# Kernel optimization log

Hardware: AMD Instinct MI355X
Metric: run time of the kernel (lower is better)

Reference implementation:

```python
import jax, jax.numpy as jnp
import numpy as np

B, L, D, H = 4, 2048, 1024, 16
DH = D // H
THETA = 100000.0


def setup_inputs() -> dict:
    key = jax.random.key(0)
    k1, k2, k3 = jax.random.split(key, 3)
    std_w = (2.0 / (D + 3 * D)) ** 0.5
    std_o = (2.0 / (D + D)) ** 0.5
    return {
        "x": jax.random.normal(k1, (B, L, D), dtype=jnp.float32),
        "W": jax.random.normal(k2, (3 * D, D), dtype=jnp.float32) * std_w,
        "Wo": jax.random.normal(k3, (D, D), dtype=jnp.float32) * std_o,
    }


def _rope(t):
    # t: [B, H, L, DH]; interleaved pair rotation as in the torch module
    pos = jnp.arange(L, dtype=jnp.float32)
    inv_freq = 1.0 / THETA ** (jnp.arange(0, DH, 2, dtype=jnp.float32) / DH)
    ang = pos[:, None] * inv_freq[None, :]            # [L, DH/2]
    cos = jnp.cos(ang)[:, :, None]                    # [L, DH/2, 1]
    sin = jnp.sin(ang)[:, :, None]
    tp = t.reshape(*t.shape[:-1], DH // 2, 2)         # pairs (x1, x2)
    x1, x2 = tp[..., 0], tp[..., 1]
    rot = jnp.stack([-x2, x1], axis=-1)               # [-x2, x1]
    out = tp * cos + rot * sin
    return out.reshape(*t.shape)


def reference(x, W, Wo):
    # fused QKV projection: weight layout is (t h d) along output dim
    qkv = jnp.einsum('bld,ed->ble', x, W)             # [B, L, 3D]
    qkv = qkv.reshape(B, L, 3, H, DH)
    qkv = jnp.transpose(qkv, (0, 3, 1, 2, 4))         # [B, H, L, 3, DH]
    Q, K, V = qkv[..., 0, :], qkv[..., 1, :], qkv[..., 2, :]
    Q, K = _rope(Q), _rope(K)
    scores = jnp.einsum('bhqd,bhkd->bhqk', Q, K) / (DH ** 0.5)
    causal = jnp.tril(jnp.ones((L, L), dtype=bool))
    scores = jnp.where(causal, scores, -jnp.inf)
    attn = jax.nn.softmax(scores, axis=-1)
    out = jnp.einsum('bhqk,bhkd->bhqd', attn, V)      # [B, H, L, DH]
    out = jnp.transpose(out, (0, 2, 1, 3)).reshape(B, L, D)
    return jnp.einsum('bld,ed->ble', out, Wo)
```

## Files before the change

### kernel.cpp

```cpp
#include <hip/hip_runtime.h>
#include <cstddef>
#include <cstdint>


typedef unsigned short u16;
typedef short bf16x8 __attribute__((ext_vector_type(8)));
typedef float f32x4 __attribute__((ext_vector_type(4)));

#define B_   4
#define L_   2048
#define H_   16
#define DH_  64
#define D_   1024
#define E3_  3072

__device__ __forceinline__ u16 f2bf(float f) {
  unsigned int u = __float_as_uint(f);
  u += 0x7fffu + ((u >> 16) & 1u);
  return (u16)(u >> 16);
}
__device__ __forceinline__ float bf2f(u16 h) {
  return __uint_as_float(((unsigned int)h) << 16);
}
__device__ __forceinline__ unsigned pk2(float a, float b) {
  return ((__float_as_uint(a) + 0x8000u) >> 16) |
         ((__float_as_uint(b) + 0x8000u) & 0xffff0000u);
}
__device__ __forceinline__ float fexp2(float x) {
#if __has_builtin(__builtin_amdgcn_exp2f)
  return __builtin_amdgcn_exp2f(x);
#else
  return exp2f(x);
#endif
}

__device__ __forceinline__ void gload_lds16(const void* g, void* l) {
  auto gp = reinterpret_cast<const uint32_t __attribute__((address_space(1)))*>(
      reinterpret_cast<uintptr_t>(g));
  auto lp = reinterpret_cast<uint32_t __attribute__((address_space(3)))*>(
      reinterpret_cast<uintptr_t>(l));
  __builtin_amdgcn_global_load_lds(gp, lp, 16, 0, 0);
}

__global__ __launch_bounds__(256) void cvt_bf16(const float* __restrict__ in,
                                                u16* __restrict__ out, int n8) {
  int i = blockIdx.x * 256 + threadIdx.x;
  if (i >= n8) return;
  const float4* p = (const float4*)in;
  float4 a = p[2 * i], b = p[2 * i + 1];
  uint4 o;
  o.x = (unsigned)f2bf(a.x) | ((unsigned)f2bf(a.y) << 16);
  o.y = (unsigned)f2bf(a.z) | ((unsigned)f2bf(a.w) << 16);
  o.z = (unsigned)f2bf(b.x) | ((unsigned)f2bf(b.y) << 16);
  o.w = (unsigned)f2bf(b.z) | ((unsigned)f2bf(b.w) << 16);
  ((uint4*)out)[i] = o;
}

template <bool OUT_BF16>
__global__ __launch_bounds__(256) void gemm_bt(const u16* __restrict__ A,
                                               const u16* __restrict__ Bm,
                                               void* __restrict__ C, int N, int K) {
  __shared__ __align__(16) u16 As[128 * 32];
  __shared__ __align__(16) u16 Bs[128 * 32];
  const int tid = threadIdx.x;
  const int lane = tid & 63, wave = tid >> 6;
  const int quad = lane >> 4, l15 = lane & 15;
  const int wm = (wave >> 1) << 6, wn = (wave & 1) << 6;
  const int m0 = blockIdx.y << 7, n0 = blockIdx.x << 7;

  f32x4 acc[4][4];
#pragma unroll
  for (int i = 0; i < 4; ++i)
#pragma unroll
    for (int j = 0; j < 4; ++j) acc[i][j] = {0.f, 0.f, 0.f, 0.f};

  const int sr = lane >> 2;
  const int sc = (lane & 3) * 8;

  for (int k0 = 0; k0 < K; k0 += 32) {
#pragma unroll
    for (int it = 0; it < 2; ++it) {
      const int chunk = wave * 2 + it;
      const int row = chunk * 16 + sr;
      gload_lds16(A + (size_t)(m0 + row) * K + k0 + sc, As + chunk * 512);
      gload_lds16(Bm + (size_t)(n0 + row) * K + k0 + sc, Bs + chunk * 512);
    }
    __syncthreads();
    bf16x8 af[4], bfr[4];
#pragma unroll
    for (int i = 0; i < 4; ++i)
      af[i] = *(const bf16x8*)(As + (wm + i * 16 + l15) * 32 + quad * 8);
#pragma unroll
    for (int j = 0; j < 4; ++j)
      bfr[j] = *(const bf16x8*)(Bs + (wn + j * 16 + l15) * 32 + quad * 8);
#pragma unroll
    for (int i = 0; i < 4; ++i)
#pragma unroll
      for (int j = 0; j < 4; ++j)
        acc[i][j] = __builtin_amdgcn_mfma_f32_16x16x32_bf16(af[i], bfr[j],
                                                            acc[i][j], 0, 0, 0);
    __syncthreads();
  }
#pragma unroll
  for (int i = 0; i < 4; ++i) {
    int row = m0 + wm + i * 16 + quad * 4;
#pragma unroll
    for (int j = 0; j < 4; ++j) {
      int col = n0 + wn + j * 16 + l15;
#pragma unroll
      for (int r = 0; r < 4; ++r) {
        if (OUT_BF16)
          ((u16*)C)[(size_t)(row + r) * N + col] = f2bf(acc[i][j][r]);
        else
          ((float*)C)[(size_t)(row + r) * N + col] = acc[i][j][r];
      }
    }
  }
}

__global__ __launch_bounds__(256) void rope_qk(u16* __restrict__ qkvb) {
  int i = blockIdx.x * 256 + threadIdx.x;
  int d2 = i & 31;
  int h  = (i >> 5) & 15;
  int t  = (i >> 9) & 1;
  int bl = i >> 10;
  int l  = bl & (L_ - 1);
  size_t off = (size_t)bl * E3_ + t * D_ + h * DH_ + d2 * 2;
  float inv = exp2f((float)d2 * -0.5190512648261504f);
  float ang = (float)l * inv;
  float sn = __sinf(ang), cs = __cosf(ang);
  unsigned int v = *(const unsigned int*)(qkvb + off);
  float x1 = bf2f((u16)(v & 0xffffu)), x2 = bf2f((u16)(v >> 16));
  float o1 = x1 * cs - x2 * sn;
  float o2 = x2 * cs + x1 * sn;
  if (t == 0) { o1 *= 0.18033688011112042f; o2 *= 0.18033688011112042f; }
  *(unsigned int*)(qkvb + off) =
      (unsigned)f2bf(o1) | ((unsigned)f2bf(o2) << 16);
}

__global__ __launch_bounds__(256) void transpose_v(const u16* __restrict__ qkvb,
                                                   u16* __restrict__ Vt) {
  __shared__ u16 tile[64 * 65];
  const int bh = blockIdx.x, b = bh >> 4, h = bh & 15;
  const int lbase = blockIdx.y << 6;
  const int tid = threadIdx.x;
#pragma unroll
  for (int i = 0; i < 16; ++i) {
    int flat = i * 256 + tid;
    int l = flat >> 6, d = flat & 63;
    tile[l * 65 + d] =
        qkvb[(size_t)(b * L_ + lbase + l) * E3_ + 2 * D_ + h * DH_ + d];
  }
  __syncthreads();
#pragma unroll
  for (int i = 0; i < 16; ++i) {
    int flat = i * 256 + tid;
    int d = flat >> 6, l = flat & 63;
    Vt[(size_t)(bh * DH_ + d) * L_ + lbase + l] = tile[l * 65 + d];
  }
}

__global__ __launch_bounds__(512) void attn(const u16* __restrict__ qkvb,
                                            const u16* __restrict__ Vt,
                                            u16* __restrict__ Ob) {
  __shared__ __align__(16) u16 Ks[64 * 72];
  __shared__ __align__(16) u16 Vs[64 * 72];
  __shared__ __align__(16) u16 Ps[8][16 * 72];
  const int bh = blockIdx.y, b = bh >> 4, h = bh & 15;
  const int pair = blockIdx.x;
  const int tid = threadIdx.x;
  const int lane = tid & 63, wave = tid >> 6, quad = lane >> 4, l15 = lane & 15;
  const int r0 = tid >> 3, c0 = (tid & 7) * 8;
  u16* pw = Ps[wave];

  bf16x8 ones;
#pragma unroll
  for (int i = 0; i < 8; ++i) ones[i] = (short)0x3F80;

  for (int a = 0; a < 2; ++a) {
    const int qbase = (a ? pair : (15 - pair)) << 7;
    const int rb = qbase + wave * 16;
    const int qg = rb + l15;

    bf16x8 qf[2];
    {
      const u16* qp = qkvb + (size_t)(b * L_ + qg) * E3_ + h * DH_;
      qf[0] = *(const bf16x8*)(qp + quad * 8);
      qf[1] = *(const bf16x8*)(qp + 32 + quad * 8);
    }

    f32x4 acc[4], lacc;
    lacc = {0.f, 0.f, 0.f, 0.f};
#pragma unroll
    for (int j = 0; j < 4; ++j) acc[j] = {0.f, 0.f, 0.f, 0.f};

    uint4 kreg, vreg;
    kreg = *(const uint4*)(qkvb + (size_t)(b * L_ + r0) * E3_ + D_ +
                           h * DH_ + c0);
    vreg = *(const uint4*)(Vt + (size_t)(bh * DH_ + r0) * L_ + c0);

    const int kend = qbase + 128;
    for (int kb = 0; kb < kend; kb += 64) {
      __syncthreads();
      *(uint4*)(Ks + r0 * 72 + c0) = kreg;
      *(uint4*)(Vs + r0 * 72 + c0) = vreg;
      __syncthreads();

      if (kb + 64 < kend) {
        kreg = *(const uint4*)(qkvb + (size_t)(b * L_ + kb + 64 + r0) * E3_ +
                               D_ + h * DH_ + c0);
        vreg = *(const uint4*)(Vt + (size_t)(bh * DH_ + r0) * L_ + kb + 64 +
                               c0);
      }

      f32x4 st[4];
#pragma unroll
      for (int t = 0; t < 4; ++t) st[t] = {0.f, 0.f, 0.f, 0.f};
      __builtin_amdgcn_s_setprio(1);
#pragma unroll
      for (int ks = 0; ks < 2; ++ks) {
        bf16x8 kf[4];
#pragma unroll
        for (int t = 0; t < 4; ++t)
          kf[t] =
              *(const bf16x8*)(Ks + (t * 16 + l15) * 72 + ks * 32 + quad * 8);
#pragma unroll
        for (int t = 0; t < 4; ++t)
          st[t] = __builtin_amdgcn_mfma_f32_16x16x32_bf16(kf[t], qf[ks],
                                                          st[t], 0, 0, 0);
      }
      __builtin_amdgcn_s_setprio(0);

      {
        const bool dg = (kb + 63 > rb);
#pragma unroll
        for (int t = 0; t < 4; ++t) {
          const int kg0 = kb + t * 16 + quad * 4;
          float p0, p1, p2, p3;
          if (dg) {
            p0 = (kg0 + 0 > qg) ? 0.f : fexp2(st[t][0]);
            p1 = (kg0 + 1 > qg) ? 0.f : fexp2(st[t][1]);
            p2 = (kg0 + 2 > qg) ? 0.f : fexp2(st[t][2]);
            p3 = (kg0 + 3 > qg) ? 0.f : fexp2(st[t][3]);
          } else {
            p0 = fexp2(st[t][0]);
            p1 = fexp2(st[t][1]);
            p2 = fexp2(st[t][2]);
            p3 = fexp2(st[t][3]);
          }
          uint2 pkd = {pk2(p0, p1), pk2(p2, p3)};
          *(uint2*)(pw + l15 * 72 + t * 16 + quad * 4) = pkd;
        }
      }
      __threadfence_block();

      __builtin_amdgcn_s_setprio(1);
#pragma unroll
      for (int ks = 0; ks < 2; ++ks) {
        bf16x8 vf[4];
#pragma unroll
        for (int j = 0; j < 4; ++j)
          vf[j] =
              *(const bf16x8*)(Vs + (j * 16 + l15) * 72 + ks * 32 + quad * 8);
        bf16x8 pf = *(const bf16x8*)(pw + l15 * 72 + ks * 32 + quad * 8);
        lacc = __builtin_amdgcn_mfma_f32_16x16x32_bf16(ones, pf, lacc,
                                                       0, 0, 0);
#pragma unroll
        for (int j = 0; j < 4; ++j)
          acc[j] = __builtin_amdgcn_mfma_f32_16x16x32_bf16(vf[j], pf,
                                                           acc[j], 0, 0, 0);
      }
      __builtin_amdgcn_s_setprio(0);
    }

    {
      const float rl = 1.0f / lacc[0];
#pragma unroll
      for (int j = 0; j < 4; ++j) {
        uint2 od = {pk2(acc[j][0] * rl, acc[j][1] * rl),
                    pk2(acc[j][2] * rl, acc[j][3] * rl)};
        *(uint2*)(pw + l15 * 72 + j * 16 + quad * 4) = od;
      }
    }
    __syncthreads();
#pragma unroll
    for (int it = 0; it < 2; ++it) {
      int unit = it * 512 + tid;
      int row = unit >> 3, ch = (unit & 7) * 8;
      *(uint4*)(Ob + (size_t)(b * L_ + qbase + row) * D_ + h * DH_ + ch) =
          *(const uint4*)(Ps[row >> 4] + (row & 15) * 72 + ch);
    }
    __syncthreads();
  }
}

extern "C" void kernel_launch(void* const* d_in, const int* in_sizes, int n_in,
                              void* d_out, int out_size, void* d_ws, size_t ws_size,
                              hipStream_t stream) {
  const float* x  = (const float*)d_in[0];
  const float* W  = (const float*)d_in[1];
  const float* Wo = (const float*)d_in[2];
  float* out = (float*)d_out;

  char* ws = (char*)d_ws;
  u16* xb   = (u16*)(ws);
  u16* Wb   = (u16*)(ws + 16777216);
  u16* Wob  = (u16*)(ws + 23068672);
  u16* qkvb = (u16*)(ws + 25165824);
  u16* Vt   = (u16*)(ws + 75497472);
  u16* Ob   = (u16*)(ws + 92274688);

  cvt_bf16<<<4096, 256, 0, stream>>>(x, xb, 1048576);
  cvt_bf16<<<1536, 256, 0, stream>>>(W, Wb, 393216);
  cvt_bf16<<<512, 256, 0, stream>>>(Wo, Wob, 131072);

  gemm_bt<true><<<dim3(E3_ / 128, (B_ * L_) / 128), 256, 0, stream>>>(
      xb, Wb, qkvb, E3_, D_);

  rope_qk<<<32768, 256, 0, stream>>>(qkvb);
  transpose_v<<<dim3(B_ * H_, L_ / 64), 256, 0, stream>>>(qkvb, Vt);

  attn<<<dim3(8, B_ * H_), 512, 0, stream>>>(qkvb, Vt, Ob);

  gemm_bt<false><<<dim3(D_ / 128, (B_ * L_) / 128), 256, 0, stream>>>(
      Ob, Wob, out, D_, D_);
}
```

Before: 280.6 us.

## Double-buffer K/V tiles with direct global-to-LDS loads and XOR swizzle

The attention kernel now stages K and V tiles straight from global memory into LDS with gload_lds16, instead of going through registers and then LDS stores. The tiles are double-buffered, so the next tile loads while the current one is used, and each iteration needs one barrier instead of two. The padded LDS layout is replaced by an XOR-swizzled 64-wide layout to avoid bank conflicts. This doubles K/V shared-memory use, which may lower occupancy, and correctness depends on the global-to-LDS loads finishing before the barrier.

Result: no change. 277.7 us (-1.0%).

```diff
diff --git a/kernel.cpp b/kernel.cpp
--- a/kernel.cpp
+++ b/kernel.cpp
@@ -163,15 +163,21 @@
 __global__ __launch_bounds__(512) void attn(const u16* __restrict__ qkvb,
                                             const u16* __restrict__ Vt,
                                             u16* __restrict__ Ob) {
-  __shared__ __align__(16) u16 Ks[64 * 72];
-  __shared__ __align__(16) u16 Vs[64 * 72];
+  __shared__ __align__(16) u16 Ks[2][64 * 64];
+  __shared__ __align__(16) u16 Vs[2][64 * 64];
   __shared__ __align__(16) u16 Ps[8][16 * 72];
   const int bh = blockIdx.y, b = bh >> 4, h = bh & 15;
   const int pair = blockIdx.x;
   const int tid = threadIdx.x;
   const int lane = tid & 63, wave = tid >> 6, quad = lane >> 4, l15 = lane & 15;
-  const int r0 = tid >> 3, c0 = (tid & 7) * 8;
   u16* pw = Ps[wave];
+
+  const int srow = wave * 8 + (lane >> 3);
+  const int sgran = (lane & 7) ^ (lane >> 3);
+  const u16* ksrc0 =
+      qkvb + (size_t)(b * L_ + srow) * E3_ + D_ + h * DH_ + sgran * 8;
+  const u16* vsrc0 = Vt + (size_t)(bh * DH_ + srow) * L_ + sgran * 8;
+  const int ldst = wave * 512;
 
   bf16x8 ones;
 #pragma unroll
@@ -194,24 +200,19 @@
 #pragma unroll
     for (int j = 0; j < 4; ++j) acc[j] = {0.f, 0.f, 0.f, 0.f};
 
-    uint4 kreg, vreg;
-    kreg = *(const uint4*)(qkvb + (size_t)(b * L_ + r0) * E3_ + D_ +
-                           h * DH_ + c0);
-    vreg = *(const uint4*)(Vt + (size_t)(bh * DH_ + r0) * L_ + c0);
+    gload_lds16(ksrc0, Ks[0] + ldst);
+    gload_lds16(vsrc0, Vs[0] + ldst);
+    __syncthreads();
 
     const int kend = qbase + 128;
-    for (int kb = 0; kb < kend; kb += 64) {
-      __syncthreads();
-      *(uint4*)(Ks + r0 * 72 + c0) = kreg;
-      *(uint4*)(Vs + r0 * 72 + c0) = vreg;
-      __syncthreads();
-
+    int cur = 0;
+    for (int kb = 0; kb < kend; kb += 64, cur ^= 1) {
       if (kb + 64 < kend) {
-        kreg = *(const uint4*)(qkvb + (size_t)(b * L_ + kb + 64 + r0) * E3_ +
-                               D_ + h * DH_ + c0);
-        vreg = *(const uint4*)(Vt + (size_t)(bh * DH_ + r0) * L_ + kb + 64 +
-                               c0);
-      }
+        gload_lds16(ksrc0 + (size_t)(kb + 64) * E3_, Ks[cur ^ 1] + ldst);
+        gload_lds16(vsrc0 + (kb + 64), Vs[cur ^ 1] + ldst);
+      }
+      const u16* kcur = Ks[cur];
+      const u16* vcur = Vs[cur];
 
       f32x4 st[4];
 #pragma unroll
@@ -222,8 +223,8 @@
         bf16x8 kf[4];
 #pragma unroll
         for (int t = 0; t < 4; ++t)
-          kf[t] =
-              *(const bf16x8*)(Ks + (t * 16 + l15) * 72 + ks * 32 + quad * 8);
+          kf[t] = *(const bf16x8*)(kcur + (t * 16 + l15) * 64 +
+                                   (((ks * 4 + quad) ^ (l15 & 7)) * 8));
 #pragma unroll
         for (int t = 0; t < 4; ++t)
           st[t] = __builtin_amdgcn_mfma_f32_16x16x32_bf16(kf[t], qf[ks],
@@ -252,7 +253,8 @@
           *(uint2*)(pw + l15 * 72 + t * 16 + quad * 4) = pkd;
         }
       }
-      __threadfence_block();
+      asm volatile("s_waitcnt lgkmcnt(0)" ::: "memory");
+      __builtin_amdgcn_sched_barrier(0);
 
       __builtin_amdgcn_s_setprio(1);
 #pragma unroll
@@ -260,8 +262,8 @@
         bf16x8 vf[4];
 #pragma unroll
         for (int j = 0; j < 4; ++j)
-          vf[j] =
-              *(const bf16x8*)(Vs + (j * 16 + l15) * 72 + ks * 32 + quad * 8);
+          vf[j] = *(const bf16x8*)(vcur + (j * 16 + l15) * 64 +
+                                   (((ks * 4 + quad) ^ (l15 & 7)) * 8));
         bf16x8 pf = *(const bf16x8*)(pw + l15 * 72 + ks * 32 + quad * 8);
         lacc = __builtin_amdgcn_mfma_f32_16x16x32_bf16(ones, pf, lacc,
                                                        0, 0, 0);
@@ -271,6 +273,8 @@
                                                            acc[j], 0, 0, 0);
       }
       __builtin_amdgcn_s_setprio(0);
+
+      __syncthreads();
     }
 
     {
```
